# Kernel optimization log

Hardware: AMD Instinct MI355X
Metric: run time of the kernel (lower is better)

Reference implementation:

```python
import jax, jax.numpy as jnp
import numpy as np

# static config (mirrors init_kwargs)
B, IMG_C, IN_C, OUT_C, S = 16, 3, 256, 512, 128
HIDDEN = IN_C                     # min(out_dim, in_dim) in DepthwiseSynthesisKernel
KGEN_IN = 32                      # (3+1)//2 * 4 * (512//128)
KSIZE = 3                         # generated depthwise kernel taps (= conv_kernel)
NUM_TAPS = KGEN_IN - 2 * KSIZE + 2  # 28, low-pass filter taps
CUTOFF, HALFWIDTH = 32.0, 7.35
CONV_CLAMP = 256.0
LRELU_GAIN = float(np.sqrt(2.0))  # bias_act def_gain for lrelu
DN = ('NCHW', 'OIHW', 'NCHW')

def _firwin(numtaps, cutoff, width, fs):
    # numpy re-implementation of scipy.signal.firwin (kaiser window, lowpass)
    nyq = fs / 2.0
    atten = 2.285 * (numtaps - 1) * np.pi * (width / nyq) + 7.95
    if atten > 50:
        beta = 0.1102 * (atten - 8.7)
    elif atten > 21:
        beta = 0.5842 * (atten - 21) ** 0.4 + 0.07886 * (atten - 21)
    else:
        beta = 0.0
    m = np.arange(numtaps) - (numtaps - 1) / 2.0
    c = cutoff / nyq
    h = c * np.sinc(c * m) * np.kaiser(numtaps, beta)
    return (h / h.sum()).astype(np.float32)

def setup_inputs():
    key = jax.random.key(0)
    ks = jax.random.split(key, 9)
    img = jax.random.normal(ks[0], (B, IMG_C, S, S), jnp.float32)
    fromrgb_w = jax.random.normal(ks[1], (IN_C, IMG_C, 1, 1), jnp.float32)
    fromrgb_b = jnp.zeros((IN_C,), jnp.float32)
    freqs = jax.random.normal(ks[2], (HIDDEN, 2), jnp.float32)
    radii = jnp.sqrt(jnp.sum(freqs ** 2, axis=1, keepdims=True))
    freqs = freqs / (radii * jnp.exp(radii ** 2) ** 0.25) * 8.0  # w0_init = 8
    phases = jax.random.uniform(ks[3], (HIDDEN,), jnp.float32) - 0.5
    hz_outdim = jax.random.normal(ks[4], (IN_C, HIDDEN), jnp.float32)
    vt_outdim = jax.random.normal(ks[5], (IN_C, HIDDEN), jnp.float32)
    gauss_sigma = jnp.ones((), jnp.float32)
    lr_weight0 = jax.random.normal(ks[6], (IN_C, IN_C, 1, 1), jnp.float32) / np.sqrt(IN_C)
    point_w = jax.random.normal(ks[7], (OUT_C, IN_C, 1, 1), jnp.float32)
    point_b = jnp.zeros((OUT_C,), jnp.float32)
    low_filter = jnp.asarray(_firwin(NUM_TAPS, CUTOFF, HALFWIDTH * 2, CUTOFF * 2 ** 1.1))
    gauss_x = jnp.arange(KGEN_IN, dtype=jnp.float32) - (KGEN_IN - 1) / 2.0
    fir = jnp.array([1.0, 3.0, 3.0, 1.0], jnp.float32)
    fir = fir / fir.sum()  # upfirdn2d.setup_filter normalization
    return dict(img=img, fromrgb_w=fromrgb_w, fromrgb_b=fromrgb_b, freqs=freqs,
                phases=phases, hz_outdim=hz_outdim, vt_outdim=vt_outdim,
                gauss_sigma=gauss_sigma, lr_weight0=lr_weight0, point_w=point_w,
                point_b=point_b, low_filter=low_filter, gauss_x=gauss_x, fir=fir)

def _conv(x, w, stride=(1, 1), pad=((0, 0), (0, 0)), groups=1):
    return jax.lax.conv_general_dilated(x, w, stride, pad,
                                        feature_group_count=groups,
                                        dimension_numbers=DN)

def _bias_act(x, b, act, gain, clamp):
    x = x + b[None, :, None, None]
    if act == 'lrelu':
        x = jnp.where(x >= 0, x, 0.2 * x)
    x = x * gain
    return jnp.clip(x, -clamp, clamp)

def _sample_weight(grid, coeff, gauss_sigma, gauss_x, low_filter):
    # grid: [HIDDEN, KGEN_IN], coeff: [IN_C, HIDDEN] -> [IN_C, KSIZE]
    basis = jnp.sin(grid * (2.0 * jnp.pi)) * np.float32(np.exp(-0.5))  # density = 1
    w = jnp.einsum('cg,ic->ig', basis, coeff) / np.float32(np.sqrt(HIDDEN))
    w = w - w.mean()
    w = w * jax.lax.rsqrt(jnp.mean(w * w, axis=0, keepdims=True) + 1e-8)
    gs = 1.0 + gauss_sigma ** 2 / 5.0
    w = w * jnp.exp(-(gauss_x ** 2) / (2.0 * gs))
    # valid 1D correlation with low-pass filter, then stride-2 pick
    w = jax.lax.conv_general_dilated(w[:, None, :], low_filter[None, None, :], (1,),
                                     [(0, 0)], dimension_numbers=('NCH', 'OIH', 'NCH'))[:, 0, :]
    return w[:, ::2]

def _forward(img, fromrgb_w, fromrgb_b, freqs, phases, hz_outdim, vt_outdim,
             gauss_sigma, lr_weight0, point_w, point_b, low_filter, gauss_x, fir):
    # fromrgb: Conv2dLayer(act='linear') applies sin() to input, then conv + bias + clamp
    x = jnp.sin(img)
    x = _conv(x, fromrgb_w * np.float32(1.0 / np.sqrt(IMG_C)))  # weight_gain 1/sqrt(in*k^2)
    x = _bias_act(x, fromrgb_b, 'linear', 1.0, CONV_CLAMP)
    # conv0_gen: generate separable depthwise kernels
    g = (jnp.arange(KGEN_IN, dtype=jnp.float32) - (KGEN_IN - 1) / 2.0) * (2.0 / (KGEN_IN + 1))
    hz = _sample_weight(freqs[:, 0:1] * g[None, :] + phases[:, None], hz_outdim,
                        gauss_sigma, gauss_x, low_filter)  # [IN_C, 3]
    vt = _sample_weight(freqs[:, 1:2] * g[None, :] + phases[:, None], vt_outdim,
                        gauss_sigma, gauss_x, low_filter)
    gdw = np.float32(1.0 / np.sqrt(KSIZE))  # Conv2dWrapper weight_gain, I=1, kHkW=3
    y = _conv(x, (vt * gdw).reshape(IN_C, 1, KSIZE, 1), pad=((1, 1), (0, 0)), groups=IN_C)
    y = _conv(y, (hz * gdw).reshape(IN_C, 1, 1, KSIZE), pad=((0, 0), (1, 1)), groups=IN_C)
    # low-rank 1x1 residual path (lr_weight0 via Conv2dWrapper: extra 1/sqrt(IN_C) gain)
    y = y + _conv(x, lr_weight0 * np.float32(1.0 / np.sqrt(IN_C)))
    # conv0_point: 1x1, lrelu, gain sqrt(2), clamp
    y = _conv(y, point_w * np.float32(1.0 / np.sqrt(IN_C)))
    y = _bias_act(y, point_b, 'lrelu', LRELU_GAIN, CONV_CLAMP)
    # FIR downsample by 2 with separable [1,3,3,1]/8 filter (upfirdn2d.downsample2d)
    fv = jnp.broadcast_to(fir.reshape(1, 1, 4, 1), (OUT_C, 1, 4, 1))
    fh = jnp.broadcast_to(fir.reshape(1, 1, 1, 4), (OUT_C, 1, 1, 4))
    y = _conv(y, fv, stride=(2, 1), pad=((1, 1), (0, 0)), groups=OUT_C)
    y = _conv(y, fh, stride=(1, 2), pad=((0, 0), (1, 1)), groups=OUT_C)
    return y  # [B, OUT_C, S//2, S//2]

def reference(img, fromrgb_w, fromrgb_b, freqs, phases, hz_outdim, vt_outdim,
              gauss_sigma, lr_weight0, point_w, point_b, low_filter, gauss_x, fir):
    return _forward(img, fromrgb_w, fromrgb_b, freqs, phases, hz_outdim, vt_outdim,
                    gauss_sigma, lr_weight0, point_w, point_b, low_filter, gauss_x, fir)
```

## Files before the change

kernel.cpp:

```cpp
#include <hip/hip_runtime.h>

typedef __attribute__((ext_vector_type(4))) float f32x4;
typedef __attribute__((ext_vector_type(8))) short s16x8;
typedef unsigned short u16;

#define KGEN 32
#define NTAPS 28

__device__ __forceinline__ float bf2f(u16 v) {
    return __uint_as_float(((unsigned)v) << 16);
}
__device__ __forceinline__ u16 f2bf(float f) {
    unsigned u = __float_as_uint(f);
    unsigned r = (u + 0x7fffu + ((u >> 16) & 1u)) >> 16;
    return (u16)r;
}

#define ASYNC_COPY16(gptr, lptr)                                               \
    __builtin_amdgcn_global_load_lds(                                          \
        (const __attribute__((address_space(1))) unsigned int*)(gptr),         \
        (__attribute__((address_space(3))) unsigned int*)(lptr), 16, 0, 0)

__global__ __launch_bounds__(256) void prep_kernel(
    const float* __restrict__ freqs, const float* __restrict__ phases,
    const float* __restrict__ hz_outdim, const float* __restrict__ vt_outdim,
    const float* __restrict__ gsig, const float* __restrict__ low_filter,
    const float* __restrict__ gauss_x, float* __restrict__ hzvt,
    const float* __restrict__ point_w, const float* __restrict__ lr_w,
    u16* __restrict__ wcat,
    const float* __restrict__ img, const float* __restrict__ frw,
    const float* __restrict__ frb, u16* __restrict__ xu)
{
    __shared__ union {
        struct {
            float basis[256][KGEN];
            float red[256];
            float colscale[KGEN];
        } g;
        float pw[256];
    } sm;

    const int bidx = blockIdx.x;
    const int t = threadIdx.x;

    if (bidx < 2) {
        const int which = bidx;
        const int i = t;
        {
            float f = freqs[i * 2 + which];
            float p = phases[i];
            #pragma unroll
            for (int j = 0; j < KGEN; j++) {
                float g = ((float)j - 15.5f) * (2.0f / 33.0f);
                sm.g.basis[i][j] = sinf((f * g + p) * 6.283185307179586f) * 0.6065306597126334f;
            }
        }
        __syncthreads();

        const float* coeff = (which == 0) ? hz_outdim : vt_outdim;
        float acc[KGEN];
        #pragma unroll
        for (int j = 0; j < KGEN; j++) acc[j] = 0.f;

        const float4* crow = (const float4*)(coeff + (size_t)i * 256);
        for (int c4 = 0; c4 < 64; c4++) {
            float4 cv = crow[c4];
            int c = c4 * 4;
            #pragma unroll
            for (int j = 0; j < KGEN; j++) {
                acc[j] += sm.g.basis[c][j] * cv.x + sm.g.basis[c + 1][j] * cv.y
                        + sm.g.basis[c + 2][j] * cv.z + sm.g.basis[c + 3][j] * cv.w;
            }
        }
        #pragma unroll
        for (int j = 0; j < KGEN; j++) acc[j] *= 0.0625f;

        float s = 0.f;
        #pragma unroll
        for (int j = 0; j < KGEN; j++) s += acc[j];
        sm.g.red[i] = s;
        __syncthreads();
        for (int st = 128; st > 0; st >>= 1) {
            if (i < st) sm.g.red[i] += sm.g.red[i + st];
            __syncthreads();
        }
        float mean = sm.g.red[0] * (1.0f / 8192.0f);
        #pragma unroll
        for (int j = 0; j < KGEN; j++) acc[j] -= mean;

        #pragma unroll
        for (int j = 0; j < KGEN; j++) sm.g.basis[i][j] = acc[j];
        __syncthreads();
        if (i < KGEN) {
            float ss = 0.f;
            for (int r = 0; r < 256; r++) { float v = sm.g.basis[r][i]; ss += v * v; }
            sm.g.colscale[i] = rsqrtf(ss * (1.0f / 256.0f) + 1e-8f);
        }
        __syncthreads();

        float sg = gsig[0];
        float gs = 1.0f + sg * sg * 0.2f;
        #pragma unroll
        for (int j = 0; j < KGEN; j++) {
            float gx = gauss_x[j];
            acc[j] = acc[j] * sm.g.colscale[j] * expf(-(gx * gx) / (2.0f * gs));
        }

        float lf[NTAPS];
        #pragma unroll
        for (int tt = 0; tt < NTAPS; tt++) lf[tt] = low_filter[tt];
        #pragma unroll
        for (int p = 0; p < 3; p++) {
            int t0 = 2 * p;
            float o = 0.f;
            #pragma unroll
            for (int tt = 0; tt < NTAPS; tt++) o += acc[t0 + tt] * lf[tt];
            hzvt[((size_t)which * 256 + i) * 3 + p] = o;
        }
    } else if (bidx < 514) {
        const int n = bidx - 2;
        const int j = t;
        sm.pw[j] = point_w[(size_t)n * 256 + j];
        __syncthreads();
        float a0 = 0.f, a1 = 0.f, a2 = 0.f, a3 = 0.f;
        for (int c = 0; c < 256; c += 4) {
            a0 += sm.pw[c + 0] * lr_w[(size_t)(c + 0) * 256 + j];
            a1 += sm.pw[c + 1] * lr_w[(size_t)(c + 1) * 256 + j];
            a2 += sm.pw[c + 2] * lr_w[(size_t)(c + 2) * 256 + j];
            a3 += sm.pw[c + 3] * lr_w[(size_t)(c + 3) * 256 + j];
        }
        float acc = (a0 + a1) + (a2 + a3);
        wcat[(size_t)n * 512 + j]       = f2bf(sm.pw[j] * 0.0625f);
        wcat[(size_t)n * 512 + 256 + j] = f2bf(acc * (1.0f / 256.0f));
    } else {
        const int pos = (bidx - 514) * 8 + (t >> 5);
        const int c0 = (t & 31) * 8;
        const int b = pos >> 14;
        const int hw = pos & 16383;

        const float* ib = img + (size_t)b * 3 * 16384 + hw;
        float s0 = sinf(ib[0]);
        float s1 = sinf(ib[16384]);
        float s2 = sinf(ib[32768]);
        const float g = 0.5773502691896258f;

        union { float4 v[6]; float f[24]; } wv;
        const float4* wp = (const float4*)(frw + (size_t)c0 * 3);
        #pragma unroll
        for (int q = 0; q < 6; q++) wv.v[q] = wp[q];

        union { u16 q[8]; s16x8 v; } ov;
        #pragma unroll
        for (int q = 0; q < 8; q++) {
            float v = (s0 * wv.f[q * 3 + 0] + s1 * wv.f[q * 3 + 1] + s2 * wv.f[q * 3 + 2]) * g
                    + frb[c0 + q];
            v = fminf(256.f, fmaxf(-256.f, v));
            ov.q[q] = f2bf(v);
        }
        *(s16x8*)(xu + (size_t)pos * 512 + 256 + c0) = ov.v;
    }
}

__global__ __launch_bounds__(256) void dw_kernel(
    u16* __restrict__ xu, const float* __restrict__ hzvt)
{
    const int t = blockIdx.x * 256 + threadIdx.x;
    const int c0 = (t & 31) * 8;
    const int pos = t >> 5;
    const int w = pos & 127;
    const int h = (pos >> 7) & 127;
    const int b = pos >> 14;

    union { float4 v[6]; float f[24]; } hzw, vtw;
    const float4* hp = (const float4*)(hzvt + (size_t)c0 * 3);
    const float4* vp = (const float4*)(hzvt + 768 + (size_t)c0 * 3);
    #pragma unroll
    for (int q = 0; q < 6; q++) { hzw.v[q] = hp[q]; vtw.v[q] = vp[q]; }

    float acc8[8];
    #pragma unroll
    for (int q = 0; q < 8; q++) acc8[q] = 0.f;

    #pragma unroll
    for (int i = 0; i < 3; i++) {
        int hh = h + i - 1;
        if (hh < 0 || hh > 127) continue;
        float hr[8];
        #pragma unroll
        for (int q = 0; q < 8; q++) hr[q] = 0.f;
        #pragma unroll
        for (int j = 0; j < 3; j++) {
            int ww = w + j - 1;
            if (ww < 0 || ww > 127) continue;
            const u16* xp = xu + ((size_t)((b * 128 + hh) * 128 + ww) * 512 + 256 + c0);
            s16x8 xv = *(const s16x8*)xp;
            #pragma unroll
            for (int q = 0; q < 8; q++) hr[q] += hzw.f[q * 3 + j] * bf2f((u16)xv[q]);
        }
        #pragma unroll
        for (int q = 0; q < 8; q++) acc8[q] += vtw.f[q * 3 + i] * hr[q];
    }

    union { u16 q[8]; s16x8 v; } ov;
    #pragma unroll
    for (int q = 0; q < 8; q++) ov.q[q] = f2bf(acc8[q] * (1.0f / 3.0f));
    *(s16x8*)(xu + (size_t)pos * 512 + c0) = ov.v;
}

__global__ __launch_bounds__(256) void gemm_kernel(
    const u16* __restrict__ xu, const u16* __restrict__ wcat,
    const float* __restrict__ point_b, u16* __restrict__ ypre, int nofs)
{
    __shared__ u16 As[128 * 64];
    __shared__ u16 Bs[128 * 64];

    const int tid = threadIdx.x;
    const int bid = blockIdx.x;
    const int ntile = (bid >> 3) & 1;
    const int mtile = (bid & 7) | ((bid >> 4) << 3);

    const int srow = tid >> 3;
    const int slot = tid & 7;
    const int ek = slot ^ (srow & 7);
    const size_t abase = (size_t)(mtile * 128 + srow) * 512 + ek * 8;
    const int nbase = nofs + ntile * 128;
    const size_t bbase = (size_t)(nbase + srow) * 512 + ek * 8;
    u16* asdst = &As[(size_t)tid * 8];
    u16* bsdst = &Bs[(size_t)tid * 8];

    const int lane = tid & 63;
    const int wave = tid >> 6;
    const int wm = (wave >> 1) * 64;
    const int wn = (wave & 1) * 64;
    const int l16 = lane & 15;
    const int lq = lane >> 4;

    f32x4 acc[4][4];
    #pragma unroll
    for (int a = 0; a < 4; a++)
        #pragma unroll
        for (int c = 0; c < 4; c++) acc[a][c] = (f32x4){0.f, 0.f, 0.f, 0.f};

    for (int kt = 0; kt < 8; kt++) {
        __syncthreads();
        const int ko = kt * 64;
        #pragma unroll
        for (int i = 0; i < 4; i++) {
            ASYNC_COPY16(xu + abase + (size_t)i * 32 * 512 + ko, asdst + i * 2048);
            ASYNC_COPY16(wcat + bbase + (size_t)i * 32 * 512 + ko, bsdst + i * 2048);
        }
        __syncthreads();

        #pragma unroll
        for (int kk = 0; kk < 2; kk++) {
            s16x8 af[4], bf[4];
            #pragma unroll
            for (int mi = 0; mi < 4; mi++) {
                const int r = wm + mi * 16 + l16;
                af[mi] = *(const s16x8*)&As[r * 64 + (((kk * 4 + lq) ^ (r & 7)) * 8)];
            }
            #pragma unroll
            for (int ni = 0; ni < 4; ni++) {
                const int r = wn + ni * 16 + l16;
                bf[ni] = *(const s16x8*)&Bs[r * 64 + (((kk * 4 + lq) ^ (r & 7)) * 8)];
            }
            #pragma unroll
            for (int mi = 0; mi < 4; mi++)
                #pragma unroll
                for (int ni = 0; ni < 4; ni++)
                    acc[mi][ni] = __builtin_amdgcn_mfma_f32_16x16x32_bf16(
                        af[mi], bf[ni], acc[mi][ni], 0, 0, 0);
        }
    }

    const int b = mtile >> 7;
    const int h = mtile & 127;
    #pragma unroll
    for (int ni = 0; ni < 4; ni++) {
        const int nl = ntile * 128 + wn + ni * 16 + l16;
        const float bias = point_b[nofs + nl];
        u16* drow = ypre + ((size_t)(b * 256 + nl) * 128 + h) * 128;
        #pragma unroll
        for (int mi = 0; mi < 4; mi++) {
            const int w0 = wm + mi * 16 + lq * 4;
            union { u16 q[4]; uint2 d; } pk;
            #pragma unroll
            for (int r = 0; r < 4; r++) {
                float v = acc[mi][ni][r] + bias;
                v = (v >= 0.f) ? v : 0.2f * v;
                v *= 1.4142135623730951f;
                v = fminf(256.f, fmaxf(-256.f, v));
                pk.q[r] = f2bf(v);
            }
            *(uint2*)(drow + w0) = pk.d;
        }
    }
}

__global__ __launch_bounds__(256) void fir_kernel(
    const u16* __restrict__ ypre, const float* __restrict__ fir,
    float* __restrict__ out, int nofs)
{
    const int bid = blockIdx.x;
    const int tid = threadIdx.x;
    const int lane = tid & 63;
    const int wave = tid >> 6;
    const int nl = bid & 255;
    const int b = bid >> 8;
    const u16* src = ypre + (size_t)(b * 256 + nl) * 16384;
    float* dst = out + (size_t)(b * 512 + nofs + nl) * 4096;

    const float f0 = fir[0], f1 = fir[1], f2 = fir[2], f3 = fir[3];

    auto hrow = [&](int r) -> float {
        if (r < 0 || r > 127) return 0.f;
        unsigned raw = *(const unsigned*)(src + (size_t)r * 128 + lane * 2);
        float y0 = bf2f((u16)(raw & 0xffffu));
        float y1 = bf2f((u16)(raw >> 16));
        float ym = __shfl_up(y1, 1u);
        if (lane == 0) ym = 0.f;
        float yp = __shfl_down(y0, 1u);
        if (lane == 63) yp = 0.f;
        return f0 * ym + f1 * y0 + f2 * y1 + f3 * yp;
    };

    const int oh0 = wave * 16;
    float A = hrow(2 * oh0 - 1);
    float Bv = hrow(2 * oh0);
    for (int oh = oh0; oh < oh0 + 16; oh++) {
        float C = hrow(2 * oh + 1);
        float D = hrow(2 * oh + 2);
        dst[oh * 64 + lane] = f0 * A + f1 * Bv + f2 * C + f3 * D;
        A = C;
        Bv = D;
    }
}

extern "C" void kernel_launch(void* const* d_in, const int* in_sizes, int n_in,
                              void* d_out, int out_size, void* d_ws, size_t ws_size,
                              hipStream_t stream)
{
    (void)in_sizes; (void)n_in; (void)out_size; (void)ws_size;
    const float* img        = (const float*)d_in[0];
    const float* fromrgb_w  = (const float*)d_in[1];
    const float* fromrgb_b  = (const float*)d_in[2];
    const float* freqs      = (const float*)d_in[3];
    const float* phases     = (const float*)d_in[4];
    const float* hz_outdim  = (const float*)d_in[5];
    const float* vt_outdim  = (const float*)d_in[6];
    const float* gsig       = (const float*)d_in[7];
    const float* lr_w       = (const float*)d_in[8];
    const float* point_w    = (const float*)d_in[9];
    const float* point_b    = (const float*)d_in[10];
    const float* low_filter = (const float*)d_in[11];
    const float* gauss_x    = (const float*)d_in[12];
    const float* fir        = (const float*)d_in[13];

    char* ws = (char*)d_ws;
    u16*   xu   = (u16*)(ws);
    u16*   ypre = (u16*)(ws + 268435456LL);
    u16*   wcat = (u16*)(ws + 402653184LL);
    float* hzvt = (float*)(ws + 403177472LL);
    float* out  = (float*)d_out;

    hipLaunchKernelGGL(prep_kernel, dim3(33282), dim3(256), 0, stream,
                       freqs, phases, hz_outdim, vt_outdim, gsig, low_filter, gauss_x, hzvt,
                       point_w, lr_w, wcat, img, fromrgb_w, fromrgb_b, xu);
    hipLaunchKernelGGL(dw_kernel, dim3(32768), dim3(256), 0, stream,
                       xu, hzvt);
    for (int half = 0; half < 2; half++) {
        hipLaunchKernelGGL(gemm_kernel, dim3(4096), dim3(256), 0, stream,
                           xu, wcat, point_b, ypre, half * 256);
        hipLaunchKernelGGL(fir_kernel, dim3(4096), dim3(256), 0, stream,
                           ypre, fir, out, half * 256);
    }
}
```

Measured before the change: 747.0 us.

## Rework fromrgb, depthwise, GEMM epilogue and FIR kernels for better reuse and coalescing

The fromrgb path now computes each pixel's sine once in shared memory and has each thread emit 32 channels using transposed weights staged in LDS. The depthwise kernel computes four adjacent output pixels per thread, reusing the six loaded input columns across them and folding the separable weights into a combined 3x3. The GEMM epilogue stages output tiles through swizzled LDS so each row is written with wide 16-byte stores. The FIR kernel splits output rows across twice as many blocks. __sinf replaces sinf, which trades some accuracy for speed.

```diff
diff --git a/kernel.cpp b/kernel.cpp
--- a/kernel.cpp
+++ b/kernel.cpp
@@ -38,6 +38,11 @@
             float colscale[KGEN];
         } g;
         float pw[256];
+        struct {
+            float sins[3][32];
+            float wT[3][264];
+            float bT[264];
+        } f;
     } sm;
 
     const int bidx = blockIdx.x;
@@ -52,7 +57,7 @@
             #pragma unroll
             for (int j = 0; j < KGEN; j++) {
                 float g = ((float)j - 15.5f) * (2.0f / 33.0f);
-                sm.g.basis[i][j] = sinf((f * g + p) * 6.283185307179586f) * 0.6065306597126334f;
+                sm.g.basis[i][j] = __sinf((f * g + p) * 6.283185307179586f) * 0.6065306597126334f;
             }
         }
         __syncthreads();
@@ -133,43 +138,56 @@
         wcat[(size_t)n * 512 + j]       = f2bf(sm.pw[j] * 0.0625f);
         wcat[(size_t)n * 512 + 256 + j] = f2bf(acc * (1.0f / 256.0f));
     } else {
-        const int pos = (bidx - 514) * 8 + (t >> 5);
-        const int c0 = (t & 31) * 8;
-        const int b = pos >> 14;
-        const int hw = pos & 16383;
-
-        const float* ib = img + (size_t)b * 3 * 16384 + hw;
-        float s0 = sinf(ib[0]);
-        float s1 = sinf(ib[16384]);
-        float s2 = sinf(ib[32768]);
-        const float g = 0.5773502691896258f;
-
-        union { float4 v[6]; float f[24]; } wv;
-        const float4* wp = (const float4*)(frw + (size_t)c0 * 3);
-        #pragma unroll
-        for (int q = 0; q < 6; q++) wv.v[q] = wp[q];
-
-        union { u16 q[8]; s16x8 v; } ov;
-        #pragma unroll
-        for (int q = 0; q < 8; q++) {
-            float v = (s0 * wv.f[q * 3 + 0] + s1 * wv.f[q * 3 + 1] + s2 * wv.f[q * 3 + 2]) * g
-                    + frb[c0 + q];
-            v = fminf(256.f, fmaxf(-256.f, v));
-            ov.q[q] = f2bf(v);
-        }
-        *(s16x8*)(xu + (size_t)pos * 512 + 256 + c0) = ov.v;
+        const int pos_base = (bidx - 514) * 32;
+        const int b = pos_base >> 14;
+        const int hw = pos_base & 16383;
+
+        if (t < 96) {
+            const int ch = t >> 5, p = t & 31;
+            sm.f.sins[ch][p] = __sinf(img[((size_t)b * 3 + ch) * 16384 + hw + p]);
+        }
+        for (int idx = t; idx < 768; idx += 256) {
+            const int c = idx / 3, k = idx - c * 3;
+            sm.f.wT[k][c + (c >> 5)] = frw[idx];
+        }
+        sm.f.bT[t + (t >> 5)] = frb[t];
+        __syncthreads();
+
+        const int p = t >> 3;
+        const int g8 = t & 7;
+        const int c0 = g8 * 32;
+        const float s0 = sm.f.sins[0][p];
+        const float s1 = sm.f.sins[1][p];
+        const float s2 = sm.f.sins[2][p];
+        const float gn = 0.5773502691896258f;
+
+        u16* dst = xu + (size_t)(pos_base + p) * 512 + 256 + c0;
+        #pragma unroll
+        for (int q0 = 0; q0 < 4; q0++) {
+            union { u16 q[8]; s16x8 v; } ov;
+            #pragma unroll
+            for (int q = 0; q < 8; q++) {
+                const int cp = c0 + q0 * 8 + q + g8;
+                float v = (s0 * sm.f.wT[0][cp] + s1 * sm.f.wT[1][cp]
+                         + s2 * sm.f.wT[2][cp]) * gn + sm.f.bT[cp];
+                v = fminf(256.f, fmaxf(-256.f, v));
+                ov.q[q] = f2bf(v);
+            }
+            *(s16x8*)(dst + q0 * 8) = ov.v;
+        }
     }
 }
 
 __global__ __launch_bounds__(256) void dw_kernel(
     u16* __restrict__ xu, const float* __restrict__ hzvt)
 {
-    const int t = blockIdx.x * 256 + threadIdx.x;
+    const int t = threadIdx.x;
     const int c0 = (t & 31) * 8;
-    const int pos = t >> 5;
-    const int w = pos & 127;
-    const int h = (pos >> 7) & 127;
-    const int b = pos >> 14;
+    const int wq = t >> 5;
+    const int pos0 = blockIdx.x * 32 + wq * 4;
+    const int w0 = pos0 & 127;
+    const int h = (pos0 >> 7) & 127;
+    const int b = pos0 >> 14;
 
     union { float4 v[6]; float f[24]; } hzw, vtw;
     const float4* hp = (const float4*)(hzvt + (size_t)c0 * 3);
@@ -177,42 +195,60 @@
     #pragma unroll
     for (int q = 0; q < 6; q++) { hzw.v[q] = hp[q]; vtw.v[q] = vp[q]; }
 
-    float acc8[8];
-    #pragma unroll
-    for (int q = 0; q < 8; q++) acc8[q] = 0.f;
+    float acc[4][8];
+    #pragma unroll
+    for (int o = 0; o < 4; o++)
+        #pragma unroll
+        for (int q = 0; q < 8; q++) acc[o][q] = 0.f;
 
     #pragma unroll
     for (int i = 0; i < 3; i++) {
         int hh = h + i - 1;
         if (hh < 0 || hh > 127) continue;
-        float hr[8];
-        #pragma unroll
-        for (int q = 0; q < 8; q++) hr[q] = 0.f;
-        #pragma unroll
-        for (int j = 0; j < 3; j++) {
-            int ww = w + j - 1;
-            if (ww < 0 || ww > 127) continue;
-            const u16* xp = xu + ((size_t)((b * 128 + hh) * 128 + ww) * 512 + 256 + c0);
-            s16x8 xv = *(const s16x8*)xp;
-            #pragma unroll
-            for (int q = 0; q < 8; q++) hr[q] += hzw.f[q * 3 + j] * bf2f((u16)xv[q]);
-        }
-        #pragma unroll
-        for (int q = 0; q < 8; q++) acc8[q] += vtw.f[q * 3 + i] * hr[q];
-    }
-
-    union { u16 q[8]; s16x8 v; } ov;
-    #pragma unroll
-    for (int q = 0; q < 8; q++) ov.q[q] = f2bf(acc8[q] * (1.0f / 3.0f));
-    *(s16x8*)(xu + (size_t)pos * 512 + c0) = ov.v;
+        float w2[3][8];
+        #pragma unroll
+        for (int q = 0; q < 8; q++) {
+            const float vq = vtw.f[q * 3 + i];
+            w2[0][q] = vq * hzw.f[q * 3 + 0];
+            w2[1][q] = vq * hzw.f[q * 3 + 1];
+            w2[2][q] = vq * hzw.f[q * 3 + 2];
+        }
+        const u16* rowp = xu + ((size_t)((b * 128 + hh) * 128) * 512) + 256 + c0;
+        #pragma unroll
+        for (int dx = 0; dx < 6; dx++) {
+            const int ww = w0 + dx - 1;
+            s16x8 xv;
+            if (ww >= 0 && ww <= 127) xv = *(const s16x8*)(rowp + (size_t)ww * 512);
+            else xv = (s16x8){0,0,0,0,0,0,0,0};
+            float xf[8];
+            #pragma unroll
+            for (int q = 0; q < 8; q++) xf[q] = bf2f((u16)xv[q]);
+            #pragma unroll
+            for (int o = 0; o < 4; o++) {
+                const int j = dx - o;
+                if (j < 0 || j > 2) continue;
+                #pragma unroll
+                for (int q = 0; q < 8; q++) acc[o][q] += w2[j][q] * xf[q];
+            }
+        }
+    }
+
+    #pragma unroll
+    for (int o = 0; o < 4; o++) {
+        union { u16 q[8]; s16x8 v; } ov;
+        #pragma unroll
+        for (int q = 0; q < 8; q++) ov.q[q] = f2bf(acc[o][q] * (1.0f / 3.0f));
+        *(s16x8*)(xu + (size_t)(pos0 + o) * 512 + c0) = ov.v;
+    }
 }
 
 __global__ __launch_bounds__(256) void gemm_kernel(
     const u16* __restrict__ xu, const u16* __restrict__ wcat,
     const float* __restrict__ point_b, u16* __restrict__ ypre, int nofs)
 {
-    __shared__ u16 As[128 * 64];
-    __shared__ u16 Bs[128 * 64];
+    __shared__ u16 smem[16384];
+    u16* As = smem;
+    u16* Bs = smem + 8192;
 
     const int tid = threadIdx.x;
     const int bid = blockIdx.x;
@@ -273,16 +309,14 @@
         }
     }
 
-    const int b = mtile >> 7;
-    const int h = mtile & 127;
+    __syncthreads();
     #pragma unroll
     for (int ni = 0; ni < 4; ni++) {
-        const int nl = ntile * 128 + wn + ni * 16 + l16;
-        const float bias = point_b[nofs + nl];
-        u16* drow = ypre + ((size_t)(b * 256 + nl) * 128 + h) * 128;
+        const int nloc = wn + ni * 16 + l16;
+        const float bias = point_b[nofs + ntile * 128 + nloc];
         #pragma unroll
         for (int mi = 0; mi < 4; mi++) {
-            const int w0 = wm + mi * 16 + lq * 4;
+            const int m0 = wm + mi * 16 + lq * 4;
             union { u16 q[4]; uint2 d; } pk;
             #pragma unroll
             for (int r = 0; r < 4; r++) {
@@ -292,8 +326,26 @@
                 v = fminf(256.f, fmaxf(-256.f, v));
                 pk.q[r] = f2bf(v);
             }
-            *(uint2*)(drow + w0) = pk.d;
-        }
+            const int chunk = m0 >> 3;
+            const int within = m0 & 7;
+            const int sl = chunk ^ (nloc & 7);
+            *(uint2*)&smem[nloc * 128 + sl * 8 + within] = pk.d;
+        }
+    }
+    __syncthreads();
+
+    const int b = mtile >> 7;
+    const int h = mtile & 127;
+    const int nl2 = tid >> 1;
+    const int halfsel = tid & 1;
+    const int nl = ntile * 128 + nl2;
+    u16* drow = ypre + ((size_t)(b * 256 + nl) * 128 + h) * 128;
+    #pragma unroll
+    for (int j = 0; j < 8; j++) {
+        const int c = halfsel * 8 + j;
+        const int sl = c ^ (nl2 & 7);
+        uint4 v = *(const uint4*)&smem[nl2 * 128 + sl * 8];
+        *(uint4*)(drow + c * 8) = v;
     }
 }
 
@@ -305,8 +357,9 @@
     const int tid = threadIdx.x;
     const int lane = tid & 63;
     const int wave = tid >> 6;
-    const int nl = bid & 255;
-    const int b = bid >> 8;
+    const int ohhalf = bid & 1;
+    const int nl = (bid >> 1) & 255;
+    const int b = bid >> 9;
     const u16* src = ypre + (size_t)(b * 256 + nl) * 16384;
     float* dst = out + (size_t)(b * 512 + nofs + nl) * 4096;
 
@@ -324,10 +377,10 @@
         return f0 * ym + f1 * y0 + f2 * y1 + f3 * yp;
     };
 
-    const int oh0 = wave * 16;
+    const int oh0 = ohhalf * 32 + wave * 8;
     float A = hrow(2 * oh0 - 1);
     float Bv = hrow(2 * oh0);
-    for (int oh = oh0; oh < oh0 + 16; oh++) {
+    for (int oh = oh0; oh < oh0 + 8; oh++) {
         float C = hrow(2 * oh + 1);
         float D = hrow(2 * oh + 2);
         dst[oh * 64 + lane] = f0 * A + f1 * Bv + f2 * C + f3 * D;
@@ -363,15 +416,15 @@
     float* hzvt = (float*)(ws + 403177472LL);
     float* out  = (float*)d_out;
 
-    hipLaunchKernelGGL(prep_kernel, dim3(33282), dim3(256), 0, stream,
+    hipLaunchKernelGGL(prep_kernel, dim3(8706), dim3(256), 0, stream,
                        freqs, phases, hz_outdim, vt_outdim, gsig, low_filter, gauss_x, hzvt,
                        point_w, lr_w, wcat, img, fromrgb_w, fromrgb_b, xu);
-    hipLaunchKernelGGL(dw_kernel, dim3(32768), dim3(256), 0, stream,
+    hipLaunchKernelGGL(dw_kernel, dim3(8192), dim3(256), 0, stream,
                        xu, hzvt);
     for (int half = 0; half < 2; half++) {
         hipLaunchKernelGGL(gemm_kernel, dim3(4096), dim3(256), 0, stream,
                            xu, wcat, point_b, ypre, half * 256);
-        hipLaunchKernelGGL(fir_kernel, dim3(4096), dim3(256), 0, stream,
+        hipLaunchKernelGGL(fir_kernel, dim3(8192), dim3(256), 0, stream,
                            ypre, fir, out, half * 256);
     }
 }
```

Measured after the change: 677.8 us. 1.1x faster.
